# Performance work log

Measured on AMD Instinct MI355X. Metric: run time of the kernel, lower is better.

The kernel has to match this reference:

```python
import jax, jax.numpy as jnp
import numpy as np

MODEL_DIM = 2048
HEAD_DIM = 64
STATE_DIM = 128
EXPAND = 2
CHUNK = 64
INNER = EXPAND * MODEL_DIM          # 4096
NHEADS = INNER // HEAD_DIM          # 64
IN_PROJ = INNER + 2 * STATE_DIM + NHEADS  # 4416
B_SZ = 2
SEQ = 4096


def segsum(x):
    """Stable segment sum: x (..., T) -> (..., T, T) with -inf above diagonal."""
    T = x.shape[-1]
    mask_strict = jnp.tril(jnp.ones((T, T), dtype=bool), -1)
    # element [d, e] = x[d] on strictly-lower triangle, 0 elsewhere
    xt = jnp.where(mask_strict, x[..., :, None], 0.0)
    seg = jnp.cumsum(xt, axis=-2)
    mask = jnp.tril(jnp.ones((T, T), dtype=bool), 0)
    return jnp.where(mask, seg, -jnp.inf)


def ssd(x, A, B, C, chunk):
    """Mamba-2 SSD. x:(b,L,h,p), A:(b,L,h), B/C:(b,L,n) shared over heads."""
    b, L, h, p = x.shape
    n = B.shape[-1]
    c = L // chunk
    x = x.reshape(b, c, chunk, h, p)
    A = A.reshape(b, c, chunk, h).transpose(0, 3, 1, 2)  # (b,h,c,l)
    B = B.reshape(b, c, chunk, n)
    C = C.reshape(b, c, chunk, n)

    A_cs = jnp.cumsum(A, axis=-1)                        # (b,h,c,l)
    Lm = jnp.exp(segsum(A))                              # (b,h,c,l,l)
    # 1. diagonal (intra-chunk) output
    Y_diag = jnp.einsum('bcln,bcsn,bhcls,bcshp->bclhp', C, B, Lm, x)
    # 2. per-chunk states
    decay_states = jnp.exp(A_cs[..., -1:] - A_cs)        # (b,h,c,l)
    states = jnp.einsum('bcln,bhcl,bclhp->bchpn', B, decay_states, x)
    states = jnp.concatenate([jnp.zeros_like(states[:, :1]), states], axis=1)
    # 3. inter-chunk recurrence
    A_chunk = jnp.pad(A_cs[..., -1], ((0, 0), (0, 0), (1, 0)))   # (b,h,c+1)
    decay_chunk = jnp.exp(segsum(A_chunk))               # (b,h,c+1,c+1)
    new_states = jnp.einsum('bhzc,bchpn->bzhpn', decay_chunk, states)
    states_prev, final_state = new_states[:, :-1], new_states[:, -1]
    # 4. state -> output
    Y_off = jnp.einsum('bcln,bchpn,bhcl->bclhp', C, states_prev, jnp.exp(A_cs))
    Y = (Y_diag + Y_off).reshape(b, L, h, p)
    return Y, final_state


def setup_inputs() -> dict:
    key = jax.random.key(0)
    ks = jax.random.split(key, 6)
    u = jax.random.normal(ks[0], (B_SZ, SEQ, MODEL_DIM), jnp.float32)
    W_in = jax.random.normal(ks[1], (IN_PROJ, MODEL_DIM), jnp.float32) * 0.02
    b_in = jnp.zeros((IN_PROJ,), jnp.float32)
    W_out = jax.random.normal(ks[2], (MODEL_DIM, INNER), jnp.float32) * 0.02
    b_out = jnp.zeros((MODEL_DIM,), jnp.float32)
    # A_log = log(uniform(1, 16)) per Mamba-2 init
    A_log = jnp.log(jax.random.uniform(ks[3], (NHEADS,), jnp.float32, 1.0, 16.0))
    # dt_bias = inv-softplus of dt ~ loguniform(1e-3, 1e-1)
    dt = jnp.exp(jax.random.uniform(ks[4], (NHEADS,), jnp.float32)
                 * (np.log(0.1) - np.log(0.001)) + np.log(0.001))
    dt = jnp.clip(dt, 1e-4, None)
    dt_bias = dt + jnp.log(-jnp.expm1(-dt))
    return {'u': u, 'W_in': W_in, 'b_in': b_in, 'W_out': W_out,
            'b_out': b_out, 'A_log': A_log, 'dt_bias': dt_bias}


def reference(u, W_in, b_in, W_out, b_out, A_log, dt_bias):
    xBCdt = u @ W_in.T + b_in                       # (b, L, IN_PROJ)
    x, Bm, Cm, dt = jnp.split(
        xBCdt, [INNER, INNER + STATE_DIM, INNER + 2 * STATE_DIM], axis=-1)
    A = -jnp.exp(A_log)                             # (h,)
    dt = jax.nn.softplus(dt + dt_bias)              # (b, L, h)
    x = x.reshape(B_SZ, SEQ, NHEADS, HEAD_DIM)
    y, final_state = ssd(x * dt[..., None], A * dt, Bm, Cm, CHUNK)
    y = y.reshape(B_SZ, SEQ, INNER)
    y = y @ W_out.T + b_out
    return y, final_state
```

## Files before the change

### kernel.cpp

```cpp
#include <hip/hip_runtime.h>
#include <hip/hip_bf16.h>

typedef __hip_bfloat16 bf16;
typedef __attribute__((ext_vector_type(8))) short short8;
typedef __attribute__((ext_vector_type(4))) float f32x4;

#define MODEL_DIM 2048
#define INNER     4096
#define NHEADS    64
#define HEAD_DIM  64
#define STATE_DIM 128
#define IN_PROJ   4416
#define NPAD      4608
#define BSZ       2
#define SEQ       4096
#define CHUNKL    64
#define NTOK      (BSZ*SEQ)
#define NCHUNK    (SEQ/CHUNKL)

#define WAITV0() asm volatile("s_waitcnt vmcnt(0)" ::: "memory")
#define BAR()    __builtin_amdgcn_s_barrier()
#define WAITLGKM() do { asm volatile("s_waitcnt lgkmcnt(0)" ::: "memory"); \
                        __builtin_amdgcn_sched_barrier(0); } while (0)

#define SWZ(x) ((x) ^ ((((x) >> 7) & 7) << 4))

static __device__ __forceinline__ void gload_lds16(const bf16* g, bf16* l) {
  __builtin_amdgcn_global_load_lds((const __attribute__((address_space(1))) void*)g,
                                   (__attribute__((address_space(3))) void*)l, 16, 0, 0);
}

static __device__ __forceinline__ unsigned lds_u32(const void* p) {
  return (unsigned)(unsigned long long)(const __attribute__((address_space(3))) char*)p;
}

static __device__ __forceinline__ short8 ds_read128(unsigned addr) {
  short8 r;
  asm volatile("ds_read_b128 %0, %1" : "=v"(r) : "v"(addr));
  return r;
}

static __device__ __forceinline__ void stage_unit(const bf16* __restrict__ P, int K,
                                                  int blockRow, int kt,
                                                  char* region, int unit, int t) {
  int o = unit * 8192 + (t << 4);
  int lb = SWZ(o);
  int row = lb >> 7, colb = lb & 127;
  gload_lds16(P + (size_t)(blockRow + row) * K + kt + (colb >> 1), (bf16*)(region + o));
}

template<int BN>
static __device__ __forceinline__ void gemm_core1(
    const bf16* __restrict__ Ag, const bf16* __restrict__ Bg,
    int K, int NT, int bm, int bn, char* lds, f32x4 (&acc)[8][BN / 64]) {
  constexpr int NR = BN / 64;
  constexpr int BB = 32768 + NR * 8192;
  const int t = threadIdx.x;
  const int lane = t & 63;
  const int wid = t >> 6, wm = wid >> 2, wn = wid & 3;
  const unsigned x16 = (unsigned)(lane & 7) << 4;
  const unsigned kb0 = (unsigned)(lane >> 4) << 4;
  const unsigned ldsB = lds_u32(lds);
  const unsigned aRow0 = (unsigned)(wm * 128 + (lane & 15)) * 128;
  const unsigned bRow0 = (unsigned)(wn * (BN / 4) + (lane & 15)) * 128;

#pragma unroll
  for (int u = 0; u < 4; ++u) stage_unit(Ag, K, bm, 0, lds, u, t);
#pragma unroll
  for (int u = 0; u < NR; ++u) stage_unit(Bg, K, bn, 0, lds + 32768, u, t);
  WAITV0();
  BAR();

  int cur = 0;
  for (int tt = 0; tt < NT; ++tt) {
    char* oth = lds + (cur ^ 1) * BB;
    const unsigned aB = ldsB + (unsigned)(cur * BB);
    const unsigned bB = aB + 32768;
    const bool st = (tt + 1 < NT);

    if (st) {
      const int kt1 = (tt + 1) * 64;
#pragma unroll
      for (int u = 0; u < 4; ++u) stage_unit(Ag, K, bm, kt1, oth, u, t);
#pragma unroll
      for (int u = 0; u < NR; ++u) stage_unit(Bg, K, bn, kt1, oth + 32768, u, t);
    }

    short8 a[8][2], b[NR][2];
#pragma unroll
    for (int mf = 0; mf < 8; ++mf)
#pragma unroll
      for (int ks = 0; ks < 2; ++ks)
        a[mf][ks] = ds_read128(aB + aRow0 + mf * 2048 + (((unsigned)(ks * 64) + kb0) ^ x16));
#pragma unroll
    for (int nf = 0; nf < NR; ++nf)
#pragma unroll
      for (int ks = 0; ks < 2; ++ks)
        b[nf][ks] = ds_read128(bB + bRow0 + nf * 2048 + (((unsigned)(ks * 64) + kb0) ^ x16));
    WAITLGKM();

    __builtin_amdgcn_s_setprio(1);
#pragma unroll
    for (int mf = 0; mf < 8; ++mf)
#pragma unroll
      for (int nf = 0; nf < NR; ++nf)
#pragma unroll
        for (int ks = 0; ks < 2; ++ks)
          acc[mf][nf] = __builtin_amdgcn_mfma_f32_16x16x32_bf16(a[mf][ks], b[nf][ks], acc[mf][nf], 0, 0, 0);
    __builtin_amdgcn_s_setprio(0);

    if (st) WAITV0();
    BAR();
    cur ^= 1;
  }
}

__global__ __launch_bounds__(512, 2)
void gemm_in256(const bf16* __restrict__ A, const bf16* __restrict__ Bw,
                const float* __restrict__ bias, bf16* __restrict__ x_bf,
                bf16* __restrict__ B_bf, bf16* __restrict__ C_bf, float* __restrict__ dtraw) {
  __shared__ char lds[2 * (32768 + 3 * 8192)];
  int nwg = gridDim.x, bid = blockIdx.x;
  int cpx = nwg >> 3;
  int sb = (bid & 7) * cpx + (bid >> 3);
  int bx = sb % (NPAD / 192), by = sb / (NPAD / 192);
  int bm = by * 256, bn = bx * 192;
  f32x4 acc[8][3] = {};
  gemm_core1<192>(A, Bw, MODEL_DIM, MODEL_DIM / 64, bm, bn, lds, acc);
  const int lane = threadIdx.x & 63, wid = threadIdx.x >> 6;
  const int wm = wid >> 2, wn = wid & 3;
#pragma unroll
  for (int mf = 0; mf < 8; ++mf)
#pragma unroll
    for (int nf = 0; nf < 3; ++nf)
#pragma unroll
      for (int r = 0; r < 4; ++r) {
        int row = bm + wm * 128 + mf * 16 + (lane >> 4) * 4 + r;
        int col = bn + wn * 48 + nf * 16 + (lane & 15);
        float v = acc[mf][nf][r] + ((col < IN_PROJ) ? bias[col] : 0.f);
        if (col < 4096)       x_bf[(size_t)row * 4096 + col]         = __float2bfloat16(v);
        else if (col < 4224)  B_bf[(size_t)row * 128 + (col - 4096)] = __float2bfloat16(v);
        else if (col < 4352)  C_bf[(size_t)row * 128 + (col - 4224)] = __float2bfloat16(v);
        else if (col < 4416)  dtraw[(size_t)row * 64 + (col - 4352)] = v;
      }
}

__global__ __launch_bounds__(512, 2)
void gemm_out256(const bf16* __restrict__ A, const bf16* __restrict__ Bw,
                 const float* __restrict__ bias, float* __restrict__ C) {
  __shared__ char lds[2 * (32768 + 4 * 8192)];
  int nwg = gridDim.x, bid = blockIdx.x;
  int cpx = nwg >> 3;
  int sb = (bid & 7) * cpx + (bid >> 3);
  int bx = sb % (MODEL_DIM / 256), by = sb / (MODEL_DIM / 256);
  int bm = by * 256, bn = bx * 256;
  f32x4 acc[8][4] = {};
  gemm_core1<256>(A, Bw, INNER, INNER / 64, bm, bn, lds, acc);
  const int lane = threadIdx.x & 63, wid = threadIdx.x >> 6;
  const int wm = wid >> 2, wn = wid & 3;
#pragma unroll
  for (int mf = 0; mf < 8; ++mf)
#pragma unroll
    for (int nf = 0; nf < 4; ++nf)
#pragma unroll
      for (int r = 0; r < 4; ++r) {
        int row = bm + wm * 128 + mf * 16 + (lane >> 4) * 4 + r;
        int col = bn + wn * 64 + nf * 16 + (lane & 15);
        C[(size_t)row * MODEL_DIM + col] = acc[mf][nf][r] + bias[col];
      }
}

__global__ __launch_bounds__(256) void conv_f32_to_bf16(const float* __restrict__ src,
                                                        bf16* __restrict__ dst, int n4) {
  int i = blockIdx.x * 256 + threadIdx.x;
  if (i >= n4) return;
  float4 v = *(const float4*)(src + (size_t)i * 4);
  bf16* d = dst + (size_t)i * 4;
  d[0] = __float2bfloat16(v.x); d[1] = __float2bfloat16(v.y);
  d[2] = __float2bfloat16(v.z); d[3] = __float2bfloat16(v.w);
}

__global__ __launch_bounds__(256) void conv_win_pad(const float* __restrict__ W,
                                                    bf16* __restrict__ dst) {
  int i = blockIdx.x * 256 + threadIdx.x;
  int row = (i * 4) >> 11;
  int col = (i * 4) & 2047;
  bf16* d = dst + (size_t)i * 4;
  if (row < IN_PROJ) {
    float4 v = *(const float4*)(W + (size_t)row * 2048 + col);
    d[0] = __float2bfloat16(v.x); d[1] = __float2bfloat16(v.y);
    d[2] = __float2bfloat16(v.z); d[3] = __float2bfloat16(v.w);
  } else {
    bf16 z = __float2bfloat16(0.f);
    d[0] = z; d[1] = z; d[2] = z; d[3] = z;
  }
}

__global__ __launch_bounds__(256)
void prep_small(const float* __restrict__ dtraw, const float* __restrict__ A_log,
                const float* __restrict__ dt_bias, float* __restrict__ dts,
                float* __restrict__ a_dt) {
  int i = blockIdx.x * 256 + threadIdx.x;
  int h = i & 63;
  float z = dtraw[i] + dt_bias[h];
  float dt = (z > 20.f) ? z : log1pf(expf(z));
  dts[i] = dt;
  a_dt[i] = -expf(A_log[h]) * dt;
}

__global__ __launch_bounds__(256)
void ssd_states_kernel(const bf16* __restrict__ x_bf, const bf16* __restrict__ B_bf,
                       const float* __restrict__ dts, const float* __restrict__ a_dt,
                       float* __restrict__ acs_g, bf16* __restrict__ states_g) {
  __shared__ bf16 xT[64 * 64];
  __shared__ bf16 BdT[128 * 64];
  __shared__ float acs_s[64];
  int blk = blockIdx.x;
  int h = blk & 63, c = (blk >> 6) & 63, b = blk >> 12;
  int t = threadIdx.x, lane = t & 63, wid = t >> 6;
  int tokBase = b * SEQ + c * 64;

  if (t < 64) {
    float v = a_dt[(size_t)(tokBase + t) * 64 + h];
#pragma unroll
    for (int d = 1; d < 64; d <<= 1) { float o = __shfl_up(v, d); if (t >= d) v += o; }
    acs_s[t] = v;
    acs_g[(((size_t)(b * 64 + c)) * 64 + h) * 64 + t] = v;
  }
  __syncthreads();
  float acs63 = acs_s[63];

#pragma unroll
  for (int i = 0; i < 2; ++i) {
    int chunk = t + i * 256;
    int l = chunk >> 3, p0 = (chunk & 7) * 8;
    float dtv = dts[(size_t)(tokBase + l) * 64 + h];
    short8 vv = *(const short8*)(x_bf + (size_t)(tokBase + l) * 4096 + h * 64 + p0);
    const bf16* pv = (const bf16*)&vv;
#pragma unroll
    for (int j = 0; j < 8; ++j)
      xT[(p0 + j) * 64 + l] = __float2bfloat16(__bfloat162float(pv[j]) * dtv);
  }
#pragma unroll
  for (int i = 0; i < 4; ++i) {
    int chunk = t + i * 256;
    int l = chunk >> 4, n0 = (chunk & 15) * 8;
    float dec = expf(acs63 - acs_s[l]);
    short8 vv = *(const short8*)(B_bf + (size_t)(tokBase + l) * 128 + n0);
    const bf16* pv = (const bf16*)&vv;
#pragma unroll
    for (int j = 0; j < 8; ++j)
      BdT[(n0 + j) * 64 + l] = __float2bfloat16(__bfloat162float(pv[j]) * dec);
  }
  __syncthreads();

  int pBase = (wid >> 1) * 32, nBase = (wid & 1) * 64;
  f32x4 acc[2][4] = {};
#pragma unroll
  for (int ks = 0; ks < 2; ++ks) {
    short8 a[2], bb[4];
#pragma unroll
    for (int mi = 0; mi < 2; ++mi)
      a[mi] = *(const short8*)(xT + (pBase + mi * 16 + (lane & 15)) * 64 + ks * 32 + (lane >> 4) * 8);
#pragma unroll
    for (int ni = 0; ni < 4; ++ni)
      bb[ni] = *(const short8*)(BdT + (nBase + ni * 16 + (lane & 15)) * 64 + ks * 32 + (lane >> 4) * 8);
#pragma unroll
    for (int mi = 0; mi < 2; ++mi)
#pragma unroll
      for (int ni = 0; ni < 4; ++ni)
        acc[mi][ni] = __builtin_amdgcn_mfma_f32_16x16x32_bf16(a[mi], bb[ni], acc[mi][ni], 0, 0, 0);
  }
  size_t sbase = ((size_t)((b * 64 + c) * 64 + h)) * 64 * 128;
#pragma unroll
  for (int mi = 0; mi < 2; ++mi)
#pragma unroll
    for (int ni = 0; ni < 4; ++ni)
#pragma unroll
      for (int r = 0; r < 4; ++r) {
        int p = pBase + mi * 16 + (lane >> 4) * 4 + r;
        int n = nBase + ni * 16 + (lane & 15);
        states_g[sbase + (size_t)p * 128 + n] = __float2bfloat16(acc[mi][ni][r]);
      }
}

__global__ __launch_bounds__(256)
void ssd_scan_kernel(bf16* __restrict__ states_g, const float* __restrict__ acs_g,
                     float* __restrict__ out_fs) {
  int blk = blockIdx.x;
  int q = blk & 3, bh = blk >> 2;
  int b = bh >> 6, h = bh & 63;
  int t = threadIdx.x;
  int eb = q * 2048 + t;
  float S[8];
#pragma unroll
  for (int i = 0; i < 8; ++i) S[i] = 0.f;
  for (int c = 0; c < 64; ++c) {
    size_t base = ((size_t)((b * 64 + c) * 64 + h)) * 8192;
    float dfac = expf(acs_g[(((size_t)(b * 64 + c)) * 64 + h) * 64 + 63]);
#pragma unroll
    for (int i = 0; i < 8; ++i) {
      int e = eb + i * 256;
      float cs = __bfloat162float(states_g[base + e]);
      states_g[base + e] = __float2bfloat16(S[i]);
      S[i] = dfac * S[i] + cs;
    }
  }
  size_t ob = (size_t)bh * 8192;
#pragma unroll
  for (int i = 0; i < 8; ++i) out_fs[ob + eb + i * 256] = S[i];
}

__global__ __launch_bounds__(256)
void ssd_out_kernel(bf16* __restrict__ x_bf, const bf16* __restrict__ B_bf,
                    const bf16* __restrict__ C_bf, const float* __restrict__ dts,
                    const float* __restrict__ acs_g, const bf16* __restrict__ states_g) {
  __shared__ bf16 Cs[64 * 128];
  __shared__ bf16 BsMs[64 * 128];
  __shared__ bf16 xT[64 * 64];
  __shared__ bf16 Sp[64 * 128];
  __shared__ float acs_s[64];
  int blk = blockIdx.x;
  int h = blk & 63, c = (blk >> 6) & 63, b = blk >> 12;
  int t = threadIdx.x, lane = t & 63, wid = t >> 6;
  int tokBase = b * SEQ + c * 64;
  size_t sbase = ((size_t)((b * 64 + c) * 64 + h)) * 8192;

  if (t < 64) acs_s[t] = acs_g[(((size_t)(b * 64 + c)) * 64 + h) * 64 + t];
#pragma unroll
  for (int i = 0; i < 4; ++i) {
    int chunk = t + i * 256;
    int l = chunk >> 4, n0 = (chunk & 15) * 8;
    *(short8*)(Cs + l * 128 + n0) = *(const short8*)(C_bf + (size_t)(tokBase + l) * 128 + n0);
    *(short8*)(BsMs + l * 128 + n0) = *(const short8*)(B_bf + (size_t)(tokBase + l) * 128 + n0);
  }
#pragma unroll
  for (int i = 0; i < 2; ++i) {
    int chunk = t + i * 256;
    int l = chunk >> 3, p0 = (chunk & 7) * 8;
    float dtv = dts[(size_t)(tokBase + l) * 64 + h];
    short8 vv = *(const short8*)(x_bf + (size_t)(tokBase + l) * 4096 + h * 64 + p0);
    const bf16* pv = (const bf16*)&vv;
#pragma unroll
    for (int j = 0; j < 8; ++j)
      xT[(p0 + j) * 64 + l] = __float2bfloat16(__bfloat162float(pv[j]) * dtv);
  }
#pragma unroll
  for (int i = 0; i < 4; ++i) {
    int chunk = t + i * 256;
    *(short8*)(Sp + chunk * 8) = *(const short8*)(states_g + sbase + chunk * 8);
  }
  __syncthreads();

  int lBase = (wid >> 1) * 32, sBase = (wid & 1) * 32;
  f32x4 g[2][2] = {};
#pragma unroll
  for (int ks = 0; ks < 4; ++ks) {
    short8 a[2], bb[2];
#pragma unroll
    for (int mi = 0; mi < 2; ++mi)
      a[mi] = *(const short8*)(Cs + (lBase + mi * 16 + (lane & 15)) * 128 + ks * 32 + (lane >> 4) * 8);
#pragma unroll
    for (int ni = 0; ni < 2; ++ni)
      bb[ni] = *(const short8*)(BsMs + (sBase + ni * 16 + (lane & 15)) * 128 + ks * 32 + (lane >> 4) * 8);
#pragma unroll
    for (int mi = 0; mi < 2; ++mi)
#pragma unroll
      for (int ni = 0; ni < 2; ++ni)
        g[mi][ni] = __builtin_amdgcn_mfma_f32_16x16x32_bf16(a[mi], bb[ni], g[mi][ni], 0, 0, 0);
  }
  __syncthreads();

  bf16* Ms = BsMs;
#pragma unroll
  for (int mi = 0; mi < 2; ++mi)
#pragma unroll
    for (int ni = 0; ni < 2; ++ni)
#pragma unroll
      for (int r = 0; r < 4; ++r) {
        int row = lBase + mi * 16 + (lane >> 4) * 4 + r;
        int col = sBase + ni * 16 + (lane & 15);
        float lm = (row >= col) ? expf(acs_s[row] - acs_s[col]) : 0.f;
        Ms[row * 64 + col] = __float2bfloat16(g[mi][ni][r] * lm);
      }
  __syncthreads();

  int pBase = (wid & 1) * 32;
  f32x4 yd[2][2] = {}, yo[2][2] = {};
#pragma unroll
  for (int ks = 0; ks < 2; ++ks) {
    short8 a[2], bb[2];
#pragma unroll
    for (int mi = 0; mi < 2; ++mi)
      a[mi] = *(const short8*)(Ms + (lBase + mi * 16 + (lane & 15)) * 64 + ks * 32 + (lane >> 4) * 8);
#pragma unroll
    for (int ni = 0; ni < 2; ++ni)
      bb[ni] = *(const short8*)(xT + (pBase + ni * 16 + (lane & 15)) * 64 + ks * 32 + (lane >> 4) * 8);
#pragma unroll
    for (int mi = 0; mi < 2; ++mi)
#pragma unroll
      for (int ni = 0; ni < 2; ++ni)
        yd[mi][ni] = __builtin_amdgcn_mfma_f32_16x16x32_bf16(a[mi], bb[ni], yd[mi][ni], 0, 0, 0);
  }
#pragma unroll
  for (int ks = 0; ks < 4; ++ks) {
    short8 a[2], bb[2];
#pragma unroll
    for (int mi = 0; mi < 2; ++mi)
      a[mi] = *(const short8*)(Cs + (lBase + mi * 16 + (lane & 15)) * 128 + ks * 32 + (lane >> 4) * 8);
#pragma unroll
    for (int ni = 0; ni < 2; ++ni)
      bb[ni] = *(const short8*)(Sp + (pBase + ni * 16 + (lane & 15)) * 128 + ks * 32 + (lane >> 4) * 8);
#pragma unroll
    for (int mi = 0; mi < 2; ++mi)
#pragma unroll
      for (int ni = 0; ni < 2; ++ni)
        yo[mi][ni] = __builtin_amdgcn_mfma_f32_16x16x32_bf16(a[mi], bb[ni], yo[mi][ni], 0, 0, 0);
  }
  __syncthreads();
#pragma unroll
  for (int mi = 0; mi < 2; ++mi)
#pragma unroll
    for (int ni = 0; ni < 2; ++ni)
#pragma unroll
      for (int r = 0; r < 4; ++r) {
        int lr = lBase + mi * 16 + (lane >> 4) * 4 + r;
        int p = pBase + ni * 16 + (lane & 15);
        float val = yd[mi][ni][r] + expf(acs_s[lr]) * yo[mi][ni][r];
        x_bf[(size_t)(tokBase + lr) * 4096 + h * 64 + p] = __float2bfloat16(val);
      }
}

extern "C" void kernel_launch(void* const* d_in, const int* in_sizes, int n_in,
                              void* d_out, int out_size, void* d_ws, size_t ws_size,
                              hipStream_t stream) {
  const float* u       = (const float*)d_in[0];
  const float* W_in    = (const float*)d_in[1];
  const float* b_in    = (const float*)d_in[2];
  const float* W_out   = (const float*)d_in[3];
  const float* b_out   = (const float*)d_in[4];
  const float* A_log   = (const float*)d_in[5];
  const float* dt_bias = (const float*)d_in[6];

  float* y_out  = (float*)d_out;
  float* fs_out = y_out + (size_t)NTOK * MODEL_DIM;

  char* ws = (char*)d_ws;
  size_t off = 0;
  auto alloc = [&](size_t bytes) { char* p = ws + off; off += (bytes + 255) & ~255ull; return p; };
  bf16*  wout_bf = (bf16*) alloc((size_t)MODEL_DIM * INNER * 2);
  bf16*  x_bf    = (bf16*) alloc((size_t)NTOK * INNER * 2);
  bf16*  B_bf    = (bf16*) alloc((size_t)NTOK * STATE_DIM * 2);
  bf16*  C_bf    = (bf16*) alloc((size_t)NTOK * STATE_DIM * 2);
  float* dtraw   = (float*)alloc((size_t)NTOK * NHEADS * 4);
  float* dts     = (float*)alloc((size_t)NTOK * NHEADS * 4);
  float* a_dt    = (float*)alloc((size_t)NTOK * NHEADS * 4);
  float* acs     = (float*)alloc((size_t)BSZ * NCHUNK * NHEADS * 64 * 4);
  char*  Q       = alloc((size_t)BSZ * NCHUNK * NHEADS * 64 * 128 * 2);
  bf16*  states  = (bf16*)Q;
  bf16*  u_bf    = (bf16*)Q;
  bf16*  win_bf  = u_bf + (size_t)NTOK * MODEL_DIM;
  (void)ws_size; (void)off; (void)in_sizes; (void)n_in; (void)out_size;

  conv_f32_to_bf16<<<dim3(16384), dim3(256), 0, stream>>>(u, u_bf, NTOK * MODEL_DIM / 4);
  conv_win_pad<<<dim3(NPAD * MODEL_DIM / 1024), dim3(256), 0, stream>>>(W_in, win_bf);
  conv_f32_to_bf16<<<dim3(8192), dim3(256), 0, stream>>>(W_out, wout_bf, MODEL_DIM * INNER / 4);

  gemm_in256<<<dim3((NTOK / 256) * (NPAD / 192)), dim3(512), 0, stream>>>(
      u_bf, win_bf, b_in, x_bf, B_bf, C_bf, dtraw);

  prep_small<<<dim3(NTOK * NHEADS / 256), dim3(256), 0, stream>>>(dtraw, A_log, dt_bias, dts, a_dt);

  ssd_states_kernel<<<dim3(BSZ * NCHUNK * NHEADS), dim3(256), 0, stream>>>(
      x_bf, B_bf, dts, a_dt, acs, states);

  ssd_scan_kernel<<<dim3(BSZ * NHEADS * 4), dim3(256), 0, stream>>>(states, acs, fs_out);

  ssd_out_kernel<<<dim3(BSZ * NCHUNK * NHEADS), dim3(256), 0, stream>>>(
      x_bf, B_bf, C_bf, dts, acs, states);

  gemm_out256<<<dim3((MODEL_DIM / 256) * (NTOK / 256)), dim3(512), 0, stream>>>(
      x_bf, wout_bf, b_out, y_out);
}
```

Baseline: 588.3 us.

## Restructure GEMM mainloop into eight-phase interleaved LDS read, stage, MFMA schedule

```diff
diff --git a/kernel.cpp b/kernel.cpp
--- a/kernel.cpp
+++ b/kernel.cpp
@@ -19,9 +19,12 @@
 #define NCHUNK    (SEQ/CHUNKL)
 
 #define WAITV0() asm volatile("s_waitcnt vmcnt(0)" ::: "memory")
+#define VMW6()   asm volatile("s_waitcnt vmcnt(6)" ::: "memory")
+#define VMW4()   asm volatile("s_waitcnt vmcnt(4)" ::: "memory")
+#define VMW3()   asm volatile("s_waitcnt vmcnt(3)" ::: "memory")
 #define BAR()    __builtin_amdgcn_s_barrier()
-#define WAITLGKM() do { asm volatile("s_waitcnt lgkmcnt(0)" ::: "memory"); \
-                        __builtin_amdgcn_sched_barrier(0); } while (0)
+#define SCHEDB() __builtin_amdgcn_sched_barrier(0)
+#define WAITLG0() do { asm volatile("s_waitcnt lgkmcnt(0)" ::: "memory"); SCHEDB(); } while (0)
 
 #define SWZ(x) ((x) ^ ((((x) >> 7) & 7) << 4))
 
@@ -49,11 +52,33 @@
   gload_lds16(P + (size_t)(blockRow + row) * K + kt + (colb >> 1), (bf16*)(region + o));
 }
 
+#define KOFF(ks) ((((unsigned)((ks) * 64)) + kb0) ^ x16)
+
+#define RD_A(dst, base, mo) do {                                                        \
+  _Pragma("unroll") for (int mf = 0; mf < 4; ++mf)                                      \
+    _Pragma("unroll") for (int ks = 0; ks < 2; ++ks)                                    \
+      dst[mf][ks] = ds_read128((base) + aRow0 + (unsigned)(((mo) + mf) * 2048) + KOFF(ks)); } while (0)
+
+#define RD_B(dst, base, no, cnt) do {                                                   \
+  _Pragma("unroll") for (int nf = 0; nf < (cnt); ++nf)                                  \
+    _Pragma("unroll") for (int ks = 0; ks < 2; ++ks)                                    \
+      dst[nf][ks] = ds_read128((base) + bRow0 + (unsigned)(((no) + (nf)) * 2048) + KOFF(ks)); } while (0)
+
+#define MM(av, bv, MB, NB, NC) do {                                                     \
+  __builtin_amdgcn_s_setprio(1);                                                        \
+  _Pragma("unroll") for (int mf = 0; mf < 4; ++mf)                                      \
+    _Pragma("unroll") for (int nf = 0; nf < (NC); ++nf)                                 \
+      _Pragma("unroll") for (int ks = 0; ks < 2; ++ks)                                  \
+        acc[(MB) + mf][(NB) + nf] = __builtin_amdgcn_mfma_f32_16x16x32_bf16(            \
+            av[mf][ks], bv[nf][ks], acc[(MB) + mf][(NB) + nf], 0, 0, 0);                \
+  __builtin_amdgcn_s_setprio(0); } while (0)
+
 template<int BN>
-static __device__ __forceinline__ void gemm_core1(
+static __device__ __forceinline__ void gemm_core8(
     const bf16* __restrict__ Ag, const bf16* __restrict__ Bg,
     int K, int NT, int bm, int bn, char* lds, f32x4 (&acc)[8][BN / 64]) {
   constexpr int NR = BN / 64;
+  constexpr int NRm2 = NR - 2;
   constexpr int BB = 32768 + NR * 8192;
   const int t = threadIdx.x;
   const int lane = t & 63;
@@ -63,55 +88,83 @@
   const unsigned ldsB = lds_u32(lds);
   const unsigned aRow0 = (unsigned)(wm * 128 + (lane & 15)) * 128;
   const unsigned bRow0 = (unsigned)(wn * (BN / 4) + (lane & 15)) * 128;
-
-#pragma unroll
-  for (int u = 0; u < 4; ++u) stage_unit(Ag, K, bm, 0, lds, u, t);
-#pragma unroll
-  for (int u = 0; u < NR; ++u) stage_unit(Bg, K, bn, 0, lds + 32768, u, t);
+  const unsigned aB0 = ldsB, bB0 = ldsB + 32768;
+  const unsigned aB1 = ldsB + BB, bB1 = aB1 + 32768;
+  char* A0w = lds;            char* B0w = lds + 32768;
+  char* A1w = lds + BB;       char* B1w = lds + BB + 32768;
+
+  short8 a[4][2], bhi[2][2], bloE[2][2], bloO[2][2];
+
+#pragma unroll
+  for (int u = 0; u < 4; ++u) stage_unit(Ag, K, bm, 0, A0w, u, t);
+#pragma unroll
+  for (int u = 0; u < NR; ++u) stage_unit(Bg, K, bn, 0, B0w, u, t);
+#pragma unroll
+  for (int u = 0; u < NR; ++u) stage_unit(Bg, K, bn, 64, B1w, u, t);
   WAITV0();
   BAR();
-
-  int cur = 0;
-  for (int tt = 0; tt < NT; ++tt) {
-    char* oth = lds + (cur ^ 1) * BB;
-    const unsigned aB = ldsB + (unsigned)(cur * BB);
-    const unsigned bB = aB + 32768;
-    const bool st = (tt + 1 < NT);
-
+  RD_B(bloE, bB0, 0, 2);
+
+  const int NIT = NT >> 1;
+  for (int it = 0; it < NIT; ++it) {
+    const bool st = (it + 1 < NIT);
+    const int kT1 = (2 * it + 1) * 64, kT2 = kT1 + 64, kT3 = kT2 + 64;
+
+    RD_A(a, aB0, 0);
+    stage_unit(Ag, K, bm, kT1, A1w, 0, t); stage_unit(Ag, K, bm, kT1, A1w, 1, t);
+    BAR(); WAITLG0();
+    MM(a, bloE, 0, 0, 2);
+    BAR();
+
+    RD_B(bhi, bB0, 2, NRm2);
+    stage_unit(Ag, K, bm, kT1, A1w, 2, t); stage_unit(Ag, K, bm, kT1, A1w, 3, t);
+    BAR(); WAITLG0();
+    MM(a, bhi, 0, 2, NRm2);
+    BAR();
+
+    RD_A(a, aB0, 4);
+    if (st) { stage_unit(Bg, K, bn, kT2, B0w, 0, t); stage_unit(Bg, K, bn, kT2, B0w, 1, t); }
+    BAR(); WAITLG0();
+    MM(a, bhi, 4, 2, NRm2);
+    VMW6(); BAR();
+
+    RD_B(bloO, bB1, 0, 2);
     if (st) {
-      const int kt1 = (tt + 1) * 64;
-#pragma unroll
-      for (int u = 0; u < 4; ++u) stage_unit(Ag, K, bm, kt1, oth, u, t);
-#pragma unroll
-      for (int u = 0; u < NR; ++u) stage_unit(Bg, K, bn, kt1, oth + 32768, u, t);
+      stage_unit(Bg, K, bn, kT2, B0w, 2, t);
+      if constexpr (NR == 4) stage_unit(Bg, K, bn, kT2, B0w, 3, t);
     }
-
-    short8 a[8][2], b[NR][2];
-#pragma unroll
-    for (int mf = 0; mf < 8; ++mf)
-#pragma unroll
-      for (int ks = 0; ks < 2; ++ks)
-        a[mf][ks] = ds_read128(aB + aRow0 + mf * 2048 + (((unsigned)(ks * 64) + kb0) ^ x16));
-#pragma unroll
-    for (int nf = 0; nf < NR; ++nf)
-#pragma unroll
-      for (int ks = 0; ks < 2; ++ks)
-        b[nf][ks] = ds_read128(bB + bRow0 + nf * 2048 + (((unsigned)(ks * 64) + kb0) ^ x16));
-    WAITLGKM();
-
-    __builtin_amdgcn_s_setprio(1);
-#pragma unroll
-    for (int mf = 0; mf < 8; ++mf)
-#pragma unroll
-      for (int nf = 0; nf < NR; ++nf)
-#pragma unroll
-        for (int ks = 0; ks < 2; ++ks)
-          acc[mf][nf] = __builtin_amdgcn_mfma_f32_16x16x32_bf16(a[mf][ks], b[nf][ks], acc[mf][nf], 0, 0, 0);
-    __builtin_amdgcn_s_setprio(0);
-
-    if (st) WAITV0();
+    BAR(); WAITLG0();
+    MM(a, bloE, 4, 0, 2);
+    if constexpr (NR == 4) VMW4(); else VMW3();
     BAR();
-    cur ^= 1;
+
+    RD_A(a, aB1, 0);
+    if (st) { stage_unit(Ag, K, bm, kT2, A0w, 0, t); stage_unit(Ag, K, bm, kT2, A0w, 1, t); }
+    BAR(); WAITLG0();
+    MM(a, bloO, 0, 0, 2);
+    BAR();
+
+    RD_B(bhi, bB1, 2, NRm2);
+    if (st) { stage_unit(Ag, K, bm, kT2, A0w, 2, t); stage_unit(Ag, K, bm, kT2, A0w, 3, t); }
+    BAR(); WAITLG0();
+    MM(a, bhi, 0, 2, NRm2);
+    BAR();
+
+    RD_A(a, aB1, 4);
+    if (st) { stage_unit(Bg, K, bn, kT3, B1w, 0, t); stage_unit(Bg, K, bn, kT3, B1w, 1, t); }
+    BAR(); WAITLG0();
+    MM(a, bhi, 4, 2, NRm2);
+    VMW6(); BAR();
+
+    if (st) RD_B(bloE, bB0, 0, 2);
+    if (st) {
+      stage_unit(Bg, K, bn, kT3, B1w, 2, t);
+      if constexpr (NR == 4) stage_unit(Bg, K, bn, kT3, B1w, 3, t);
+    }
+    BAR(); WAITLG0();
+    MM(a, bloO, 4, 0, 2);
+    if constexpr (NR == 4) VMW4(); else VMW3();
+    BAR();
   }
 }
 
@@ -126,7 +179,7 @@
   int bx = sb % (NPAD / 192), by = sb / (NPAD / 192);
   int bm = by * 256, bn = bx * 192;
   f32x4 acc[8][3] = {};
-  gemm_core1<192>(A, Bw, MODEL_DIM, MODEL_DIM / 64, bm, bn, lds, acc);
+  gemm_core8<192>(A, Bw, MODEL_DIM, MODEL_DIM / 64, bm, bn, lds, acc);
   const int lane = threadIdx.x & 63, wid = threadIdx.x >> 6;
   const int wm = wid >> 2, wn = wid & 3;
 #pragma unroll
@@ -155,7 +208,7 @@
   int bx = sb % (MODEL_DIM / 256), by = sb / (MODEL_DIM / 256);
   int bm = by * 256, bn = bx * 256;
   f32x4 acc[8][4] = {};
-  gemm_core1<256>(A, Bw, INNER, INNER / 64, bm, bn, lds, acc);
+  gemm_core8<256>(A, Bw, INNER, INNER / 64, bm, bn, lds, acc);
   const int lane = threadIdx.x & 63, wid = threadIdx.x >> 6;
   const int wm = wid >> 2, wn = wid & 3;
 #pragma unroll
```

Result: slower. 786.0 us (+33.6%).
